# Kernel optimization log

Hardware: AMD Instinct MI355X
Metric: run time of the kernel (lower is better)

The kernel has to match this reference:

```python
import jax, jax.numpy as jnp
import numpy as np

TEMPERATURE = 0.1


def setup_inputs() -> dict:
    key = jax.random.key(0)
    # Scale by 0.03 so exp((z/T)@(z/T).T) stays finite in fp32 (module uses
    # an unstabilized exp-sum-log, and the diagonal is ||z||^2 / T^2).
    z = jax.random.normal(key, (16384, 128), dtype=jnp.float32) * 0.03
    return {"z": z}


def reference(z) -> jnp.ndarray:
    n = z.shape[0]
    zs = z / TEMPERATURE                      # [N, d]
    a = zs @ zs.T                             # [N, N] self-similarity
    # Faithful to the original: -log(sum(exp(a), axis=1) / N), then mean.
    l = -jnp.log(jnp.exp(a).sum(axis=1) / n)  # [N]
    return l.mean()
```

## Files before the change

kernel.cpp:

```cpp
#include <hip/hip_runtime.h>
#include <stdint.h>

#define NROW 16384
#define DDIM 128
#define ROWB 256

constexpr int NB     = 64;
constexpr int NJT    = NROW / NB;
constexpr int CHUNK  = 8;
constexpr int NBLK   = 2112;

typedef __bf16 bf16x8 __attribute__((ext_vector_type(8)));
typedef float  f32x4  __attribute__((ext_vector_type(4)));
typedef int    i32x4  __attribute__((ext_vector_type(4)));

typedef const uint32_t __attribute__((address_space(1)))* gptr_t;
typedef uint32_t __attribute__((address_space(3)))*       lptr_t;

__device__ __forceinline__ unsigned short f2bf(float x) {
  union { float f; uint32_t u; } c; c.f = x;
  uint32_t u = c.u + 0x7fffu + ((c.u >> 16) & 1u);
  return (unsigned short)(u >> 16);
}

__device__ __forceinline__ int Sfun(int k) {
  const int q = k >> 2, r = k & 3;
  return 2 * q * (q + 1) + r * (q + 1);
}

__global__ __launch_bounds__(256) void prep_kernel(const float* __restrict__ z,
                                                   unsigned short* __restrict__ zs,
                                                   float* __restrict__ s,
                                                   float* __restrict__ out) {
  const float SC = 12.011224087864498f;
  int t = blockIdx.x * 256 + threadIdx.x;
  float4 v = reinterpret_cast<const float4*>(z)[t];
  ushort4 o;
  o.x = f2bf(v.x * SC); o.y = f2bf(v.y * SC);
  o.z = f2bf(v.z * SC); o.w = f2bf(v.w * SC);
  reinterpret_cast<ushort4*>(zs)[t] = o;
  if (t < NROW) s[t] = 0.0f;
  if (t == 0) out[0] = 9.704060527839234f;
}

__global__ __launch_bounds__(256, 2) void gemm_exp_kernel(const unsigned short* __restrict__ zs,
                                                          float* __restrict__ s) {
  __shared__ __align__(16) char smem[2 * NB * ROWB + 4 * CHUNK * 64 * 4];
  float* csm = (float*)(smem + 2 * NB * ROWB);
  const int tid  = threadIdx.x;
  const int lane = tid & 63;
  const int wid  = tid >> 6;

  int I, c;
  {
    const int bid = blockIdx.x;
    const int m = NBLK - bid;
    int k = (int)sqrtf(8.0f * (float)m);
    if (k > 128) k = 128;
    if (k < 1) k = 1;
    while (Sfun(k) < m) ++k;
    while (k > 1 && Sfun(k - 1) >= m) --k;
    I = 128 - k;
    c = bid - (NBLK - Sfun(k));
  }
  const int mI     = NJT - 2 * I;
  const int jt0    = 2 * I + CHUNK * c;
  const int JT_blk = min(CHUNK, mI - CHUNK * c);

  const int rowBase = I * 128 + wid * 32;
  const char* zb = (const char*)zs;
  const int kb = (lane >> 4) << 4;

  const char* rq[4];
  {
    const int r = lane & 15;
#pragma unroll
    for (int ks = 0; ks < 4; ++ks)
      rq[ks] = smem + r * 256 + ((ks * 64 + kb) ^ (r << 4));
  }
  const int dBase = wid * 4096 + lane * 16;
  int sOff[4];
#pragma unroll
  for (int i_ = 0; i_ < 4; ++i_) {
    const int db  = dBase + i_ * 1024;
    const int r_  = db >> 8;
    const int cb_ = db & 0xF0;
    sOff[i_] = (jt0 * NB + r_) * ROWB + (cb_ ^ ((r_ & 15) << 4));
  }

#define STAGE(P)                                                               \
  {                                                                            \
    _Pragma("unroll")                                                          \
    for (int i_ = 0; i_ < 4; ++i_) {                                           \
      __builtin_amdgcn_global_load_lds((gptr_t)(zb + sOff[i_]),                \
          (lptr_t)(smem + (P) + dBase + i_ * 1024), 16, 0, 0);                 \
      sOff[i_] += NB * ROWB;                                                   \
    }                                                                          \
  }

  STAGE(0);

  bf16x8 afrag[2][4];
  {
    const int r0 = rowBase + (lane & 15);
#pragma unroll
    for (int mf = 0; mf < 2; ++mf)
#pragma unroll
      for (int ks = 0; ks < 4; ++ks) {
        i32x4 raw = *reinterpret_cast<const i32x4*>(
            zb + (size_t)(r0 + mf * 16) * ROWB + ks * 64 + kb);
        afrag[mf][ks] = __builtin_bit_cast(bf16x8, raw);
      }
  }

  f32x4 rsv[2];
  float cs[4];
  rsv[0] = (f32x4){0.f, 0.f, 0.f, 0.f};
  rsv[1] = (f32x4){0.f, 0.f, 0.f, 0.f};
#pragma unroll
  for (int nf = 0; nf < 4; ++nf) cs[nf] = 0.0f;
  const f32x4 kZ = {0.f, 0.f, 0.f, 0.f};

#define COMPUTE(P, kk)                                                         \
  {                                                                            \
    f32x4 acc[2][4];                                                           \
    __builtin_amdgcn_s_setprio(1);                                             \
    _Pragma("unroll")                                                          \
    for (int ks = 0; ks < 4; ++ks) {                                           \
      bf16x8 bfr[4];                                                           \
      _Pragma("unroll")                                                        \
      for (int nf = 0; nf < 4; ++nf)                                           \
        bfr[nf] = __builtin_bit_cast(bf16x8,                                   \
            *reinterpret_cast<const i32x4*>(rq[ks] + nf * 4096 + (P)));        \
      if (ks == 0) {                                                           \
        _Pragma("unroll")                                                      \
        for (int mf = 0; mf < 2; ++mf)                                         \
          _Pragma("unroll")                                                    \
          for (int nf = 0; nf < 4; ++nf)                                       \
            acc[mf][nf] = __builtin_amdgcn_mfma_f32_16x16x32_bf16(             \
                afrag[mf][0], bfr[nf], kZ, 0, 0, 0);                           \
      } else {                                                                 \
        _Pragma("unroll")                                                      \
        for (int mf = 0; mf < 2; ++mf)                                         \
          _Pragma("unroll")                                                    \
          for (int nf = 0; nf < 4; ++nf)                                       \
            acc[mf][nf] = __builtin_amdgcn_mfma_f32_16x16x32_bf16(             \
                afrag[mf][ks], bfr[nf], acc[mf][nf], 0, 0, 0);                 \
      }                                                                        \
    }                                                                          \
    __builtin_amdgcn_s_setprio(0);                                             \
    _Pragma("unroll")                                                          \
    for (int mf = 0; mf < 2; ++mf)                                             \
      _Pragma("unroll")                                                        \
      for (int nf = 0; nf < 4; ++nf) {                                         \
        f32x4 a4 = acc[mf][nf];                                                \
        f32x4 ev;                                                              \
        ev[0] = __builtin_amdgcn_exp2f(a4[0]);                                 \
        ev[1] = __builtin_amdgcn_exp2f(a4[1]);                                 \
        ev[2] = __builtin_amdgcn_exp2f(a4[2]);                                 \
        ev[3] = __builtin_amdgcn_exp2f(a4[3]);                                 \
        rsv[mf] += ev;                                                         \
        cs[nf] += (ev[0] + ev[1]) + (ev[2] + ev[3]);                           \
      }                                                                        \
    _Pragma("unroll")                                                          \
    for (int nf = 0; nf < 4; ++nf) {                                           \
      float v = cs[nf];                                                        \
      v += __shfl_xor(v, 16);                                                  \
      v += __shfl_xor(v, 32);                                                  \
      if (lane < 16) csm[wid * (CHUNK * 64) + (kk) * 64 + nf * 16 + lane] = v; \
      cs[nf] = 0.0f;                                                           \
    }                                                                          \
  }

  int k = 0;
#pragma unroll 1
  for (; k + 2 <= JT_blk; k += 2) {
    STAGE(16384);
    asm volatile("s_waitcnt vmcnt(4)" ::: "memory");
    __builtin_amdgcn_s_barrier();
    COMPUTE(0, k);
    __builtin_amdgcn_s_barrier();

    if (k + 2 < JT_blk) {
      STAGE(0);
      asm volatile("s_waitcnt vmcnt(4)" ::: "memory");
    } else {
      asm volatile("s_waitcnt vmcnt(0)" ::: "memory");
    }
    __builtin_amdgcn_s_barrier();
    COMPUTE(16384, k + 1);
    __builtin_amdgcn_s_barrier();
  }
  if (k < JT_blk) {
    asm volatile("s_waitcnt vmcnt(0)" ::: "memory");
    __builtin_amdgcn_s_barrier();
    COMPUTE(0, k);
    __builtin_amdgcn_s_barrier();
  }
#undef STAGE
#undef COMPUTE

#pragma unroll
  for (int mf = 0; mf < 2; ++mf)
#pragma unroll
    for (int r = 0; r < 4; ++r) {
      float v = rsv[mf][r];
      v += __shfl_xor(v, 1);
      v += __shfl_xor(v, 2);
      v += __shfl_xor(v, 4);
      v += __shfl_xor(v, 8);
      if ((lane & 15) == 0) {
        const int row = rowBase + mf * 16 + ((lane >> 4) << 2) + r;
        atomicAdd(&s[row], v);
      }
    }

  __syncthreads();
  {
    const int colBase0 = jt0 * NB;
    const int diagEnd  = (I + 1) * 128;
    const int ncol     = JT_blk * NB;
#pragma unroll
    for (int k4 = 0; k4 < 2; ++k4) {
      const int idx = k4 * 256 + tid;
      if (idx < ncol) {
        const int col = colBase0 + idx;
        if (col >= diagEnd) {
          float sum = csm[idx] + csm[CHUNK * 64 + idx]
                    + csm[2 * CHUNK * 64 + idx] + csm[3 * CHUNK * 64 + idx];
          atomicAdd(&s[col], sum);
        }
      }
    }
  }
}

__global__ __launch_bounds__(256) void reduce_kernel(const float* __restrict__ s,
                                                     float* __restrict__ out) {
  const int tid  = threadIdx.x;
  const int lane = tid & 63;
  const int wid  = tid >> 6;
  float v = __log2f(s[blockIdx.x * 256 + tid]);
#pragma unroll
  for (int m = 32; m >= 1; m >>= 1) v += __shfl_xor(v, m);
  __shared__ float ws[4];
  if (lane == 0) ws[wid] = v;
  __syncthreads();
  if (tid == 0) {
    const float t = ws[0] + ws[1] + ws[2] + ws[3];
    atomicAdd(out, -4.2307473367321867e-5f * t);
  }
}

extern "C" void kernel_launch(void* const* d_in, const int* in_sizes, int n_in,
                              void* d_out, int out_size, void* d_ws, size_t ws_size,
                              hipStream_t stream) {
  const float* z = (const float*)d_in[0];
  unsigned short* zs = (unsigned short*)d_ws;
  float* s = (float*)((char*)d_ws + (size_t)NROW * DDIM * 2);
  float* out = (float*)d_out;

  prep_kernel<<<dim3(NROW * DDIM / 4 / 256), dim3(256), 0, stream>>>(z, zs, s, out);
  gemm_exp_kernel<<<dim3(NBLK), dim3(256), 0, stream>>>(zs, s);
  reduce_kernel<<<dim3(64), dim3(256), 0, stream>>>(s, out);
}
```

Before: 64.90 us.

## Software-pipeline MFMA of next tile with exp/sum epilogue of previous tile

Splits the per-tile compute into an MFMA phase and an exp/reduction phase, and uses two accumulator sets so the MFMAs of tile t+1 are issued alongside the exp2 and sums of tile t. The aim is to hide the transcendental and reduction latency behind matrix-core work. The cost is doubled accumulator registers, which may reduce occupancy. The loop structure now assumes JT_blk is even and at least 2 (there is no odd-count tail), which could be wrong for some blocks.

```diff
diff --git a/kernel.cpp b/kernel.cpp
--- a/kernel.cpp
+++ b/kernel.cpp
@@ -113,6 +113,8 @@
       }
   }
 
+  STAGE(16384);
+
   f32x4 rsv[2];
   float cs[4];
   rsv[0] = (f32x4){0.f, 0.f, 0.f, 0.f};
@@ -121,10 +123,10 @@
   for (int nf = 0; nf < 4; ++nf) cs[nf] = 0.0f;
   const f32x4 kZ = {0.f, 0.f, 0.f, 0.f};
 
-#define COMPUTE(P, kk)                                                         \
-  {                                                                            \
-    f32x4 acc[2][4];                                                           \
-    __builtin_amdgcn_s_setprio(1);                                             \
+  f32x4 accA[2][4], accB[2][4];
+
+#define MFMA_TILE(P, ACC)                                                      \
+  {                                                                            \
     _Pragma("unroll")                                                          \
     for (int ks = 0; ks < 4; ++ks) {                                           \
       bf16x8 bfr[4];                                                           \
@@ -132,28 +134,25 @@
       for (int nf = 0; nf < 4; ++nf)                                           \
         bfr[nf] = __builtin_bit_cast(bf16x8,                                   \
             *reinterpret_cast<const i32x4*>(rq[ks] + nf * 4096 + (P)));        \
-      if (ks == 0) {                                                           \
+      _Pragma("unroll")                                                        \
+      for (int mf = 0; mf < 2; ++mf)                                           \
         _Pragma("unroll")                                                      \
-        for (int mf = 0; mf < 2; ++mf)                                         \
-          _Pragma("unroll")                                                    \
-          for (int nf = 0; nf < 4; ++nf)                                       \
-            acc[mf][nf] = __builtin_amdgcn_mfma_f32_16x16x32_bf16(             \
-                afrag[mf][0], bfr[nf], kZ, 0, 0, 0);                           \
-      } else {                                                                 \
-        _Pragma("unroll")                                                      \
-        for (int mf = 0; mf < 2; ++mf)                                         \
-          _Pragma("unroll")                                                    \
-          for (int nf = 0; nf < 4; ++nf)                                       \
-            acc[mf][nf] = __builtin_amdgcn_mfma_f32_16x16x32_bf16(             \
-                afrag[mf][ks], bfr[nf], acc[mf][nf], 0, 0, 0);                 \
-      }                                                                        \
+        for (int nf = 0; nf < 4; ++nf)                                         \
+          ACC[mf][nf] = (ks == 0)                                              \
+              ? __builtin_amdgcn_mfma_f32_16x16x32_bf16(                       \
+                    afrag[mf][0], bfr[nf], kZ, 0, 0, 0)                        \
+              : __builtin_amdgcn_mfma_f32_16x16x32_bf16(                       \
+                    afrag[mf][ks], bfr[nf], ACC[mf][nf], 0, 0, 0);             \
     }                                                                          \
-    __builtin_amdgcn_s_setprio(0);                                             \
+  }
+
+#define EXP_ACC(ACC)                                                           \
+  {                                                                            \
     _Pragma("unroll")                                                          \
     for (int mf = 0; mf < 2; ++mf)                                             \
       _Pragma("unroll")                                                        \
       for (int nf = 0; nf < 4; ++nf) {                                         \
-        f32x4 a4 = acc[mf][nf];                                                \
+        f32x4 a4 = ACC[mf][nf];                                                \
         f32x4 ev;                                                              \
         ev[0] = __builtin_amdgcn_exp2f(a4[0]);                                 \
         ev[1] = __builtin_amdgcn_exp2f(a4[1]);                                 \
@@ -162,6 +161,10 @@
         rsv[mf] += ev;                                                         \
         cs[nf] += (ev[0] + ev[1]) + (ev[2] + ev[3]);                           \
       }                                                                        \
+  }
+
+#define FLUSH(kk)                                                              \
+  {                                                                            \
     _Pragma("unroll")                                                          \
     for (int nf = 0; nf < 4; ++nf) {                                           \
       float v = cs[nf];                                                        \
@@ -172,33 +175,54 @@
     }                                                                          \
   }
 
-  int k = 0;
+  asm volatile("s_waitcnt vmcnt(4)" ::: "memory");
+  __builtin_amdgcn_s_barrier();
+  __builtin_amdgcn_s_setprio(1);
+  MFMA_TILE(0, accA);
+  __builtin_amdgcn_s_setprio(0);
+  __builtin_amdgcn_s_barrier();
+
 #pragma unroll 1
-  for (; k + 2 <= JT_blk; k += 2) {
-    STAGE(16384);
+  for (int t = 1; t + 1 < JT_blk; t += 2) {
+    STAGE(0);
     asm volatile("s_waitcnt vmcnt(4)" ::: "memory");
     __builtin_amdgcn_s_barrier();
-    COMPUTE(0, k);
-    __builtin_amdgcn_s_barrier();
-
-    if (k + 2 < JT_blk) {
-      STAGE(0);
+    __builtin_amdgcn_s_setprio(1);
+    MFMA_TILE(16384, accB);
+    EXP_ACC(accA);
+    __builtin_amdgcn_s_setprio(0);
+    FLUSH(t - 1);
+    __builtin_amdgcn_s_barrier();
+
+    if (t + 2 < JT_blk) {
+      STAGE(16384);
       asm volatile("s_waitcnt vmcnt(4)" ::: "memory");
     } else {
       asm volatile("s_waitcnt vmcnt(0)" ::: "memory");
     }
     __builtin_amdgcn_s_barrier();
-    COMPUTE(16384, k + 1);
-    __builtin_amdgcn_s_barrier();
-  }
-  if (k < JT_blk) {
-    asm volatile("s_waitcnt vmcnt(0)" ::: "memory");
-    __builtin_amdgcn_s_barrier();
-    COMPUTE(0, k);
-    __builtin_amdgcn_s_barrier();
-  }
+    __builtin_amdgcn_s_setprio(1);
+    MFMA_TILE(0, accA);
+    EXP_ACC(accB);
+    __builtin_amdgcn_s_setprio(0);
+    FLUSH(t);
+    __builtin_amdgcn_s_barrier();
+  }
+
+  asm volatile("s_waitcnt vmcnt(0)" ::: "memory");
+  __builtin_amdgcn_s_barrier();
+  __builtin_amdgcn_s_setprio(1);
+  MFMA_TILE(16384, accB);
+  EXP_ACC(accA);
+  __builtin_amdgcn_s_setprio(0);
+  FLUSH(JT_blk - 2);
+  __builtin_amdgcn_s_barrier();
+  EXP_ACC(accB);
+  FLUSH(JT_blk - 1);
 #undef STAGE
-#undef COMPUTE
+#undef MFMA_TILE
+#undef EXP_ACC
+#undef FLUSH
 
 #pragma unroll
   for (int mf = 0; mf < 2; ++mf)
```

Measured after the change: 80.39 us. 1.24x slower.
